# Optimization experiments

Hardware: AMD Instinct MI355X
Metric: run time of the kernel (lower is better)

The kernel has to match this reference:

```python
import jax, jax.numpy as jnp
import numpy as np

B, C, H, W = 16, 3, 384, 1280
EPS = 1e-7


def setup_inputs() -> dict:
    key = jax.random.key(0)
    k1, k2, k3, k4 = jax.random.split(key, 4)
    source_image = jax.random.normal(k1, (B, C, H, W), jnp.float32)
    depth_map = jax.random.uniform(k2, (B, 1, H, W), jnp.float32, minval=0.1, maxval=80.0)
    pose = 0.05 * jax.random.normal(k3, (B, 6), jnp.float32)
    # realistic KITTI-style pinhole intrinsics, per-batch mild perturbation
    base = jnp.array([[0.58 * W, 0.0, 0.5 * W],
                      [0.0, 1.92 * H, 0.5 * H],
                      [0.0, 0.0, 1.0]], jnp.float32)
    noise = 1.0 + 0.01 * jax.random.normal(k4, (B, 3, 3), jnp.float32)
    intrinsic = base[None] * noise  # zero entries stay zero -> invertible
    return {"source_image": source_image, "depth_map": depth_map,
            "pose": pose, "intrinsic": intrinsic}


def rot_from_axisangle(aa):
    # aa: [B,3] -> [B,3,3] (Rodrigues)
    theta = jnp.linalg.norm(aa, axis=-1, keepdims=True)  # [B,1]
    axis = aa / (theta + EPS)
    c = jnp.cos(theta)
    s = jnp.sin(theta)
    t = 1.0 - c
    x, y, z = axis[:, 0:1], axis[:, 1:2], axis[:, 2:3]
    row0 = jnp.concatenate([t * x * x + c, t * x * y - s * z, t * z * x + s * y], axis=1)
    row1 = jnp.concatenate([t * x * y + s * z, t * y * y + c, t * y * z - s * x], axis=1)
    row2 = jnp.concatenate([t * z * x - s * y, t * y * z + s * x, t * z * z + c], axis=1)
    return jnp.stack([row0, row1, row2], axis=1)  # [B,3,3]


def bilinear_grid_sample(img, gx, gy):
    # img: [B,C,H,W]; gx,gy: [B,H,W] in [-1,1]; align_corners=True, padding zeros
    Bc, Cc, Hc, Wc = img.shape
    x = (gx + 1.0) * 0.5 * (Wc - 1)
    y = (gy + 1.0) * 0.5 * (Hc - 1)
    x0 = jnp.floor(x)
    y0 = jnp.floor(y)
    x1 = x0 + 1.0
    y1 = y0 + 1.0
    wx1 = x - x0
    wx0 = 1.0 - wx1
    wy1 = y - y0
    wy0 = 1.0 - wy1
    imgf = img.reshape(Bc, Cc, Hc * Wc)

    def gather(xi, yi):
        inb = ((xi >= 0) & (xi <= Wc - 1) & (yi >= 0) & (yi <= Hc - 1)).astype(img.dtype)
        xc = jnp.clip(xi, 0, Wc - 1).astype(jnp.int32)
        yc = jnp.clip(yi, 0, Hc - 1).astype(jnp.int32)
        idx = (yc * Wc + xc).reshape(Bc, 1, -1)
        vals = jnp.take_along_axis(imgf, jnp.broadcast_to(idx, (Bc, Cc, idx.shape[-1])), axis=2)
        return vals.reshape(Bc, Cc, Hc, Wc) * inb[:, None]

    out = (gather(x0, y0) * (wx0 * wy0)[:, None]
           + gather(x1, y0) * (wx1 * wy0)[:, None]
           + gather(x0, y1) * (wx0 * wy1)[:, None]
           + gather(x1, y1) * (wx1 * wy1)[:, None])
    return out


def reference(source_image, depth_map, pose, intrinsic):
    Bb, _, Hh, Ww = depth_map.shape
    # pixel grid, homogeneous [H,W,3] = (x, y, 1)
    ys, xs = jnp.meshgrid(jnp.arange(Hh, dtype=depth_map.dtype),
                          jnp.arange(Ww, dtype=depth_map.dtype), indexing='ij')
    pix = jnp.stack([xs, ys, jnp.ones_like(xs)], axis=-1)  # [H,W,3]
    # backproject: K^{-1} @ pix * depth
    inv_K = jnp.linalg.inv(intrinsic)  # [B,3,3]
    cam = jnp.einsum('bij,hwj->bhwi', inv_K, pix)  # [B,H,W,3]
    frustum = cam * jnp.transpose(depth_map, (0, 2, 3, 1))  # [B,H,W,3]
    # rigid transform
    R = rot_from_axisangle(pose[:, :3])  # [B,3,3]
    t = pose[:, 3:]  # [B,3]
    points = jnp.einsum('bij,bhwj->bhwi', R, frustum) + t[:, None, None, :]
    # project with K
    coord = jnp.einsum('bij,bhwj->bhwi', intrinsic, points)  # [B,H,W,3]
    z = coord[..., 2] + EPS
    px = coord[..., 0] / z
    py = coord[..., 1] / z
    gx = px / (Ww - 1) * 2.0 - 1.0
    gy = py / (Hh - 1) * 2.0 - 1.0
    return bilinear_grid_sample(source_image, gx, gy)
```

## Files before the change

### kernel.cpp

```cpp
#include <hip/hip_runtime.h>

#define B_ 16
#define C_ 3
#define H_ 384
#define W_ 1280
#define HW_ (H_*W_)
#define EPS_ 1e-7f
#define ROWS_ 8

__device__ __forceinline__ void mat3mul(const float* A, const float* Bm, float* C) {
  #pragma unroll
  for (int i = 0; i < 3; i++)
    #pragma unroll
    for (int j = 0; j < 3; j++)
      C[i*3+j] = A[i*3+0]*Bm[0*3+j] + A[i*3+1]*Bm[1*3+j] + A[i*3+2]*Bm[2*3+j];
}

__device__ void compute_MT(const float* __restrict__ pose,
                           const float* __restrict__ intr,
                           int b, float* M, float* T)
{
  float K[9];
  #pragma unroll
  for (int i = 0; i < 9; i++) K[i] = intr[b*9 + i];
  float aa0 = pose[b*6 + 0], aa1 = pose[b*6 + 1], aa2 = pose[b*6 + 2];
  float t0  = pose[b*6 + 3], t1  = pose[b*6 + 4], t2  = pose[b*6 + 5];

  float theta = sqrtf(aa0*aa0 + aa1*aa1 + aa2*aa2);
  float invn  = 1.0f / (theta + EPS_);
  float x = aa0*invn, y = aa1*invn, z = aa2*invn;
  float c = cosf(theta), s = sinf(theta), t = 1.0f - c;
  float R[9] = {
    t*x*x + c,   t*x*y - s*z, t*z*x + s*y,
    t*x*y + s*z, t*y*y + c,   t*y*z - s*x,
    t*z*x - s*y, t*y*z + s*x, t*z*z + c
  };

  float a = K[0], bb = K[1], cc = K[2];
  float d = K[3], e  = K[4], f  = K[5];
  float g = K[6], h  = K[7], ii = K[8];
  float A0 = e*ii - f*h, A1 = f*g - d*ii, A2 = d*h - e*g;
  float id = 1.0f / (a*A0 + bb*A1 + cc*A2);
  float iK[9] = {
    A0*id, (cc*h - bb*ii)*id, (bb*f - cc*e)*id,
    A1*id, (a*ii - cc*g)*id,  (cc*d - a*f)*id,
    A2*id, (bb*g - a*h)*id,   (a*e  - bb*d)*id
  };

  float KR[9];
  mat3mul(K, R, KR);
  mat3mul(KR, iK, M);
  T[0] = K[0]*t0 + K[1]*t1 + K[2]*t2;
  T[1] = K[3]*t0 + K[4]*t1 + K[5]*t2;
  T[2] = K[6]*t0 + K[7]*t1 + K[8]*t2;
}

__global__ __launch_bounds__(256) void warp_kernel(
    const float* __restrict__ src,
    const float* __restrict__ depth,
    const float* __restrict__ pose,
    const float* __restrict__ intr,
    float* __restrict__ out)
{
  __shared__ float sp[12];
  int b = blockIdx.z;
  if (threadIdx.x == 0) {
    float M[9], T[3];
    compute_MT(pose, intr, b, M, T);
    #pragma unroll
    for (int i = 0; i < 9; i++) sp[i] = M[i];
    #pragma unroll
    for (int i = 0; i < 3; i++) sp[9 + i] = T[i];
  }
  __syncthreads();
  float m00 = sp[0], m01 = sp[1], m02 = sp[2];
  float m10 = sp[3], m11 = sp[4], m12 = sp[5];
  float m20 = sp[6], m21 = sp[7], m22 = sp[8];
  float T0  = sp[9], T1  = sp[10], T2 = sp[11];

  int x    = blockIdx.x * 256 + threadIdx.x;
  int row0 = blockIdx.y * ROWS_;
  float xf = (float)x;

  float ax = m00*xf + m02;
  float bx = m10*xf + m12;
  float cxk = m20*xf + m22;

  size_t sb = (size_t)b * C_ * HW_;
  const float* s0 = src + sb;
  const float* s1 = s0 + HW_;
  const float* s2 = s1 + HW_;

  for (int r = 0; r < ROWS_; r++) {
    int i = row0 + r;
    float yf = (float)i;
    size_t pix = (size_t)b * HW_ + (size_t)i * W_ + x;

    float d = __builtin_nontemporal_load(&depth[pix]);

    float cx = (m01*yf + ax)*d + T0;
    float cy = (m11*yf + bx)*d + T1;
    float cz = (m21*yf + cxk)*d + T2;
    float zz = cz + EPS_;
    float inv = 1.0f / zz;
    float px = cx * inv;
    float py = cy * inv;

    float x0f = floorf(px), y0f = floorf(py);
    float x1f = x0f + 1.0f, y1f = y0f + 1.0f;
    float wx1 = px - x0f, wx0 = 1.0f - wx1;
    float wy1 = py - y0f, wy0 = 1.0f - wy1;

    float mx0 = (x0f >= 0.0f && x0f <= (float)(W_-1)) ? 1.0f : 0.0f;
    float mx1 = (x1f >= 0.0f && x1f <= (float)(W_-1)) ? 1.0f : 0.0f;
    float my0 = (y0f >= 0.0f && y0f <= (float)(H_-1)) ? 1.0f : 0.0f;
    float my1 = (y1f >= 0.0f && y1f <= (float)(H_-1)) ? 1.0f : 0.0f;

    int xc0 = (int)fminf(fmaxf(x0f, 0.0f), (float)(W_-1));
    int xc1 = (int)fminf(fmaxf(x1f, 0.0f), (float)(W_-1));
    int yc0 = (int)fminf(fmaxf(y0f, 0.0f), (float)(H_-1));
    int yc1 = (int)fminf(fmaxf(y1f, 0.0f), (float)(H_-1));

    int i00 = yc0*W_ + xc0;
    int i01 = yc0*W_ + xc1;
    int i10 = yc1*W_ + xc0;
    int i11 = yc1*W_ + xc1;

    float w00 = wx0*wy0*mx0*my0;
    float w01 = wx1*wy0*mx1*my0;
    float w10 = wx0*wy1*mx0*my1;
    float w11 = wx1*wy1*mx1*my1;

    size_t op = (size_t)i * W_ + x;
    float v0 = s0[i00]*w00 + s0[i01]*w01 + s0[i10]*w10 + s0[i11]*w11;
    float v1 = s1[i00]*w00 + s1[i01]*w01 + s1[i10]*w10 + s1[i11]*w11;
    float v2 = s2[i00]*w00 + s2[i01]*w01 + s2[i10]*w10 + s2[i11]*w11;
    __builtin_nontemporal_store(v0, &out[sb + op]);
    __builtin_nontemporal_store(v1, &out[sb + HW_ + op]);
    __builtin_nontemporal_store(v2, &out[sb + 2*(size_t)HW_ + op]);
  }
}

extern "C" void kernel_launch(void* const* d_in, const int* in_sizes, int n_in,
                              void* d_out, int out_size, void* d_ws, size_t ws_size,
                              hipStream_t stream) {
  const float* src   = (const float*)d_in[0];
  const float* depth = (const float*)d_in[1];
  const float* pose  = (const float*)d_in[2];
  const float* intr  = (const float*)d_in[3];
  float* out = (float*)d_out;

  dim3 grid(W_ / 256, H_ / ROWS_, B_);
  warp_kernel<<<grid, 256, 0, stream>>>(src, depth, pose, intr, out);
}
```

Before: 259.2 us.

## Use paired 8-byte gathers for bilinear taps and one pixel per thread

Each bilinear sample now fetches its horizontal neighbour pair with one 8-byte load per row and channel instead of two scalar loads. At the right image edge the pair base is clamped, and the weights are remapped onto the loaded pair so clamped or masked taps still line up. The grid is flattened to one pixel per thread over HW by batch, which drops the 8-row loop and the nontemporal depth load. This halves gather instruction count, but 8-byte loads may be misaligned and the block count grows eightfold, with more per-block setup for the matrix.

Result: faster. 238.9 us (-7.8%).

```diff
diff --git a/kernel.cpp b/kernel.cpp
--- a/kernel.cpp
+++ b/kernel.cpp
@@ -6,7 +6,14 @@
 #define W_ 1280
 #define HW_ (H_*W_)
 #define EPS_ 1e-7f
-#define ROWS_ 8
+
+typedef float v2f __attribute__((ext_vector_type(2)));
+
+__device__ __forceinline__ v2f load2(const float* p) {
+  v2f r;
+  __builtin_memcpy(&r, p, 8);
+  return r;
+}
 
 __device__ __forceinline__ void mat3mul(const float* A, const float* Bm, float* C) {
   #pragma unroll
@@ -63,7 +70,7 @@
     float* __restrict__ out)
 {
   __shared__ float sp[12];
-  int b = blockIdx.z;
+  int b = blockIdx.y;
   if (threadIdx.x == 0) {
     float M[9], T[3];
     compute_MT(pose, intr, b, M, T);
@@ -78,67 +85,71 @@
   float m20 = sp[6], m21 = sp[7], m22 = sp[8];
   float T0  = sp[9], T1  = sp[10], T2 = sp[11];
 
-  int x    = blockIdx.x * 256 + threadIdx.x;
-  int row0 = blockIdx.y * ROWS_;
-  float xf = (float)x;
+  int p = blockIdx.x * 256 + threadIdx.x;
+  int j = p % W_;
+  int i = p / W_;
 
-  float ax = m00*xf + m02;
-  float bx = m10*xf + m12;
-  float cxk = m20*xf + m22;
+  float d  = depth[(size_t)b * HW_ + p];
+  float xf = (float)j, yf = (float)i;
+
+  float cx = (m00*xf + m01*yf + m02)*d + T0;
+  float cy = (m10*xf + m11*yf + m12)*d + T1;
+  float cz = (m20*xf + m21*yf + m22)*d + T2;
+  float inv = 1.0f / (cz + EPS_);
+  float px = cx * inv;
+  float py = cy * inv;
+
+  float x0f = floorf(px), y0f = floorf(py);
+  float x1f = x0f + 1.0f, y1f = y0f + 1.0f;
+  float wx1 = px - x0f, wx0 = 1.0f - wx1;
+  float wy1 = py - y0f, wy0 = 1.0f - wy1;
+
+  float mx0 = (x0f >= 0.0f && x0f <= (float)(W_-1)) ? 1.0f : 0.0f;
+  float mx1 = (x1f >= 0.0f && x1f <= (float)(W_-1)) ? 1.0f : 0.0f;
+  float my0 = (y0f >= 0.0f && y0f <= (float)(H_-1)) ? 1.0f : 0.0f;
+  float my1 = (y1f >= 0.0f && y1f <= (float)(H_-1)) ? 1.0f : 0.0f;
+
+  int xc0 = (int)fminf(fmaxf(x0f, 0.0f), (float)(W_-1));
+  int xc1 = (int)fminf(fmaxf(x1f, 0.0f), (float)(W_-1));
+  int yc0 = (int)fminf(fmaxf(y0f, 0.0f), (float)(H_-1));
+  int yc1 = (int)fminf(fmaxf(y1f, 0.0f), (float)(H_-1));
+
+  float w00 = wx0*wy0*mx0*my0;
+  float w01 = wx1*wy0*mx1*my0;
+  float w10 = wx0*wy1*mx0*my1;
+  float w11 = wx1*wy1*mx1*my1;
+
+  int base = xc0 < (W_-2) ? xc0 : (W_-2);
+  bool s0 = (xc0 == base);
+  bool s1 = (xc1 == base + 1);
+  float wax = (s0 ? w00 : 0.0f) + (s1 ? 0.0f : w01);
+  float way = (s0 ? 0.0f : w00) + (s1 ? w01 : 0.0f);
+  float wbx = (s0 ? w10 : 0.0f) + (s1 ? 0.0f : w11);
+  float wby = (s0 ? 0.0f : w10) + (s1 ? w11 : 0.0f);
+
+  int rb0 = yc0*W_ + base;
+  int rb1 = yc1*W_ + base;
 
   size_t sb = (size_t)b * C_ * HW_;
-  const float* s0 = src + sb;
-  const float* s1 = s0 + HW_;
-  const float* s2 = s1 + HW_;
+  size_t op = (size_t)p;
+  const float* s0p = src + sb;
+  const float* s1p = s0p + HW_;
+  const float* s2p = s1p + HW_;
 
-  for (int r = 0; r < ROWS_; r++) {
-    int i = row0 + r;
-    float yf = (float)i;
-    size_t pix = (size_t)b * HW_ + (size_t)i * W_ + x;
+  v2f a0 = load2(s0p + rb0);
+  v2f b0 = load2(s0p + rb1);
+  v2f a1 = load2(s1p + rb0);
+  v2f b1 = load2(s1p + rb1);
+  v2f a2 = load2(s2p + rb0);
+  v2f b2 = load2(s2p + rb1);
 
-    float d = __builtin_nontemporal_load(&depth[pix]);
+  float v0 = a0.x*wax + a0.y*way + b0.x*wbx + b0.y*wby;
+  float v1 = a1.x*wax + a1.y*way + b1.x*wbx + b1.y*wby;
+  float v2 = a2.x*wax + a2.y*way + b2.x*wbx + b2.y*wby;
 
-    float cx = (m01*yf + ax)*d + T0;
-    float cy = (m11*yf + bx)*d + T1;
-    float cz = (m21*yf + cxk)*d + T2;
-    float zz = cz + EPS_;
-    float inv = 1.0f / zz;
-    float px = cx * inv;
-    float py = cy * inv;
-
-    float x0f = floorf(px), y0f = floorf(py);
-    float x1f = x0f + 1.0f, y1f = y0f + 1.0f;
-    float wx1 = px - x0f, wx0 = 1.0f - wx1;
-    float wy1 = py - y0f, wy0 = 1.0f - wy1;
-
-    float mx0 = (x0f >= 0.0f && x0f <= (float)(W_-1)) ? 1.0f : 0.0f;
-    float mx1 = (x1f >= 0.0f && x1f <= (float)(W_-1)) ? 1.0f : 0.0f;
-    float my0 = (y0f >= 0.0f && y0f <= (float)(H_-1)) ? 1.0f : 0.0f;
-    float my1 = (y1f >= 0.0f && y1f <= (float)(H_-1)) ? 1.0f : 0.0f;
-
-    int xc0 = (int)fminf(fmaxf(x0f, 0.0f), (float)(W_-1));
-    int xc1 = (int)fminf(fmaxf(x1f, 0.0f), (float)(W_-1));
-    int yc0 = (int)fminf(fmaxf(y0f, 0.0f), (float)(H_-1));
-    int yc1 = (int)fminf(fmaxf(y1f, 0.0f), (float)(H_-1));
-
-    int i00 = yc0*W_ + xc0;
-    int i01 = yc0*W_ + xc1;
-    int i10 = yc1*W_ + xc0;
-    int i11 = yc1*W_ + xc1;
-
-    float w00 = wx0*wy0*mx0*my0;
-    float w01 = wx1*wy0*mx1*my0;
-    float w10 = wx0*wy1*mx0*my1;
-    float w11 = wx1*wy1*mx1*my1;
-
-    size_t op = (size_t)i * W_ + x;
-    float v0 = s0[i00]*w00 + s0[i01]*w01 + s0[i10]*w10 + s0[i11]*w11;
-    float v1 = s1[i00]*w00 + s1[i01]*w01 + s1[i10]*w10 + s1[i11]*w11;
-    float v2 = s2[i00]*w00 + s2[i01]*w01 + s2[i10]*w10 + s2[i11]*w11;
-    __builtin_nontemporal_store(v0, &out[sb + op]);
-    __builtin_nontemporal_store(v1, &out[sb + HW_ + op]);
-    __builtin_nontemporal_store(v2, &out[sb + 2*(size_t)HW_ + op]);
-  }
+  __builtin_nontemporal_store(v0, &out[sb + op]);
+  __builtin_nontemporal_store(v1, &out[sb + HW_ + op]);
+  __builtin_nontemporal_store(v2, &out[sb + 2*(size_t)HW_ + op]);
 }
 
 extern "C" void kernel_launch(void* const* d_in, const int* in_sizes, int n_in,
@@ -150,6 +161,6 @@
   const float* intr  = (const float*)d_in[3];
   float* out = (float*)d_out;
 
-  dim3 grid(W_ / 256, H_ / ROWS_, B_);
+  dim3 grid(HW_ / 256, B_);
   warp_kernel<<<grid, 256, 0, stream>>>(src, depth, pose, intr, out);
 }
```
